# Optimization experiments

Hardware: AMD Instinct MI355X
Metric: run time of the kernel (lower is better)

Reference implementation:

```python
import jax, jax.numpy as jnp
import numpy as np

N = 500000      # nodes
E = 1250000     # edges
S = 50000       # subgraphs
G = 64          # graphs
D = 64          # hidden dim (M_in = M_out = 64)
NLAYERS = 5


def setup_inputs() -> dict:
    key = jax.random.key(0)
    ks = jax.random.split(key, 24)

    def p(k, shape):
        return jax.random.normal(k, shape, dtype=jnp.float32) * 0.05

    return {
        "z": jax.random.randint(ks[0], (N,), 0, 100),
        "edge_index": jax.random.randint(ks[1], (2, E), 0, N),
        "node_to_subgraph": jax.random.randint(ks[2], (N,), 0, S),
        "subgraph_to_graph": jax.random.randint(ks[3], (S,), 0, G),
        # per-layer params (stacked over the 5 conv layers)
        "z_tables": p(ks[4], (NLAYERS, 100, D)),      # Embedding(100, 64) x5
        "tf_W": p(ks[5], (NLAYERS - 1, D, 2 * D)),    # Linear(128, 64) for layers 1..4
        "tf_b": p(ks[6], (NLAYERS - 1, D)),
        "ggc_W": p(ks[7], (NLAYERS, D, D)),           # GatedGraphConv weight[0]
        "gru_wih": p(ks[8], (NLAYERS, 3 * D, D)),
        "gru_whh": p(ks[9], (NLAYERS, 3 * D, D)),
        "gru_bih": p(ks[10], (NLAYERS, 3 * D)),
        "gru_bhh": p(ks[11], (NLAYERS, 3 * D)),
        # head
        "fc1_W": p(ks[12], (32, D)), "fc1_b": p(ks[13], (32,)),
        "fc2_W": p(ks[14], (16, 32)), "fc2_b": p(ks[15], (16,)),
        "fc3_W": p(ks[16], (1, 16)), "fc3_b": p(ks[17], (1,)),
    }


def reference(z, edge_index, node_to_subgraph, subgraph_to_graph,
              z_tables, tf_W, tf_b, ggc_W,
              gru_wih, gru_whh, gru_bih, gru_bhh,
              fc1_W, fc1_b, fc2_W, fc2_b, fc3_W, fc3_b):
    src, dst = edge_index[0], edge_index[1]
    x = None
    for layer in range(NLAYERS):
        ze = z_tables[layer][z]                      # [N, 64] embedding lookup
        if x is None:
            x = ze
        else:
            x = jnp.concatenate([x, ze], axis=-1) @ tf_W[layer - 1].T + tf_b[layer - 1]
        # GatedGraphConv with num_layers=1: m = x @ W; add-aggregate; GRUCell update
        m = x @ ggc_W[layer]                          # [N, 64]
        agg = jax.ops.segment_sum(m[src], dst, num_segments=N)  # scatter-add to dst
        gi = agg @ gru_wih[layer].T + gru_bih[layer]  # [N, 192]
        gh = x @ gru_whh[layer].T + gru_bhh[layer]    # [N, 192]
        ir, iz, inn = jnp.split(gi, 3, axis=-1)
        hr, hz, hn = jnp.split(gh, 3, axis=-1)
        r = jax.nn.sigmoid(ir + hr)
        u = jax.nn.sigmoid(iz + hz)
        n = jnp.tanh(inn + r * hn)
        x = (1.0 - u) * n + u * x
    # subgraph pooling ('mean' branch actually does global_add_pool)
    x = jax.ops.segment_sum(x, node_to_subgraph, num_segments=S)   # [S, 64]
    # graph pooling (y_ndim == 1)
    x = jax.ops.segment_sum(x, subgraph_to_graph, num_segments=G)  # [G, 64]
    x = jax.nn.elu(x @ fc1_W.T + fc1_b)
    x = jax.nn.elu(x @ fc2_W.T + fc2_b)
    return x @ fc3_W.T + fc3_b                        # [G, 1]
```

## Files before the change

### kernel.cpp

```cpp
#include <hip/hip_runtime.h>
#include <hip/hip_bf16.h>

#define NN 500000
#define EE 1250000
#define NP 501760
#define NBLK 489
#define GCAP 16384

typedef __attribute__((ext_vector_type(8))) short bf16x8;
typedef __attribute__((ext_vector_type(4))) float f32x4;

__device__ __forceinline__ float ngnn97_bf2f(unsigned short u) {
  return __uint_as_float(((unsigned int)u) << 16);
}
__device__ __forceinline__ unsigned short ngnn97_f2bf(float f) {
  union { __hip_bfloat16 b; unsigned short u; } cv;
  cv.b = __float2bfloat16(f);
  return cv.u;
}
__device__ __forceinline__ void ngnn97_acc8(uint4 u, float* lo, float* hi) {
  lo[0] += __uint_as_float(u.x << 16); hi[0] += __uint_as_float(u.x & 0xFFFF0000u);
  lo[1] += __uint_as_float(u.y << 16); hi[1] += __uint_as_float(u.y & 0xFFFF0000u);
  lo[2] += __uint_as_float(u.z << 16); hi[2] += __uint_as_float(u.z & 0xFFFF0000u);
  lo[3] += __uint_as_float(u.w << 16); hi[3] += __uint_as_float(u.w & 0xFFFF0000u);
}

__global__ void ngnn97_code(float* __restrict__ out, float v) {
  if (threadIdx.x < 64) out[threadIdx.x] = v;
}

__global__ __launch_bounds__(256) void ngnn97_pre(
    const float* __restrict__ ggc, const float* __restrict__ wih,
    const float* __restrict__ whh, const float* __restrict__ bih,
    const float* __restrict__ bhh, const float* __restrict__ tfW,
    const float* __restrict__ ztab,
    unsigned short* __restrict__ Ubt, float* __restrict__ Ub,
    unsigned short* __restrict__ Vbt, unsigned short* __restrict__ ztabh) {
  int idx = blockIdx.x * 256 + threadIdx.x;
  if (idx < 163840) {
    int l = idx >> 15, r = idx & 32767;
    int n = r >> 7, k = r & 127;
    float v = 0.f;
    if (k < 64) {
      if (n < 192) {
        const float* gp = ggc + l * 4096 + k * 64;
        const float* wp = wih + l * 12288 + n * 64;
        float acc = 0.f;
#pragma unroll
        for (int t2 = 0; t2 < 64; t2++) acc = fmaf(gp[t2], wp[t2], acc);
        v = acc;
      }
    } else {
      int k2 = k - 64;
      if (n < 128) v = whh[l * 12288 + n * 64 + k2];
      else if (n >= 192) v = whh[l * 12288 + (n - 64) * 64 + k2];
    }
    Ubt[idx] = ngnn97_f2bf(v);
  } else if (idx < 196608) {
    int i2 = idx - 163840;
    Vbt[i2] = ngnn97_f2bf(tfW[i2]);
  } else if (idx < 197888) {
    int i2 = idx - 196608;
    int l = i2 >> 8, j = i2 & 255;
    float v;
    if (j < 128)      v = bih[l * 192 + j] + bhh[l * 192 + j];
    else if (j < 192) v = bih[l * 192 + j];
    else              v = bhh[l * 192 + j - 64];
    Ub[i2] = v;
  } else if (idx < 229888) {
    int i2 = idx - 197888;
    ztabh[i2] = ngnn97_f2bf(ztab[i2]);
  }
}

__global__ __launch_bounds__(256) void ngnn97_hist(const int* __restrict__ dst, int* __restrict__ counts) {
  int e = blockIdx.x * 256 + threadIdx.x;
  if (e < EE) atomicAdd(&counts[dst[e]], 1);
}

__global__ __launch_bounds__(256) void ngnn97_red(const int* __restrict__ counts, int* __restrict__ bsum) {
  __shared__ int s[256];
  int t = threadIdx.x, base = blockIdx.x * 1024;
  int v = 0;
#pragma unroll
  for (int i = 0; i < 4; i++) v += counts[base + t + i * 256];
  s[t] = v; __syncthreads();
  for (int o = 128; o > 0; o >>= 1) { if (t < o) s[t] += s[t + o]; __syncthreads(); }
  if (t == 0) bsum[blockIdx.x] = s[0];
}

__global__ __launch_bounds__(512) void ngnn97_scan1(const int* __restrict__ bsum, int* __restrict__ boff) {
  __shared__ int s[512];
  int t = threadIdx.x;
  int v = (t < NBLK) ? bsum[t] : 0;
  s[t] = v; __syncthreads();
  for (int o = 1; o < 512; o <<= 1) {
    int a = (t >= o) ? s[t - o] : 0;
    __syncthreads(); s[t] += a; __syncthreads();
  }
  if (t < NBLK) boff[t] = s[t] - v;
}

__global__ __launch_bounds__(256) void ngnn97_scan2(const int* __restrict__ counts, const int* __restrict__ boff,
                                                    int* __restrict__ row_ptr, int* __restrict__ cursor) {
  __shared__ int s[256];
  int t = threadIdx.x, base = blockIdx.x * 1024;
  int4 c = *(const int4*)(counts + base + t * 4);
  int tsum = c.x + c.y + c.z + c.w;
  s[t] = tsum; __syncthreads();
  for (int o = 1; o < 256; o <<= 1) {
    int a = (t >= o) ? s[t - o] : 0;
    __syncthreads(); s[t] += a; __syncthreads();
  }
  int off = boff[blockIdx.x] + s[t] - tsum;
  int4 r;
  r.x = off; r.y = off + c.x; r.z = off + c.x + c.y; r.w = off + c.x + c.y + c.z;
  *(int4*)(row_ptr + base + t * 4) = r;
  *(int4*)(cursor + base + t * 4) = r;
}

__global__ __launch_bounds__(256) void ngnn97_fill(const int* __restrict__ src, const int* __restrict__ dst,
                                                   int* __restrict__ cursor, int* __restrict__ srcs) {
  int e = blockIdx.x * 256 + threadIdx.x;
  if (e < EE) {
    int pos = atomicAdd(&cursor[dst[e]], 1);
    srcs[pos] = src[e];
  }
}

__global__ __launch_bounds__(256) void ngnn97_g8(const int* __restrict__ n2s, const int* __restrict__ s2g,
                                                 unsigned char* __restrict__ g8) {
  int idx = blockIdx.x * 256 + threadIdx.x;
  if (idx < NN) g8[idx] = (unsigned char)s2g[n2s[idx]];
}

__global__ __launch_bounds__(256) void ngnn97_bucket(const unsigned char* __restrict__ g8,
                                                     int* __restrict__ gcur, int* __restrict__ nlist) {
  __shared__ int hcnt[64];
  __shared__ int hbase[64];
  int t = threadIdx.x;
  int base = blockIdx.x * 1024;
  if (t < 64) hcnt[t] = 0;
  __syncthreads();
#pragma unroll
  for (int i = 0; i < 4; i++) {
    int node = base + i * 256 + t;
    if (node < NN) atomicAdd(&hcnt[g8[node]], 1);
  }
  __syncthreads();
  if (t < 64) {
    int c = hcnt[t];
    hbase[t] = (c > 0) ? atomicAdd(&gcur[t], c) : 0;
    hcnt[t] = 0;
  }
  __syncthreads();
#pragma unroll
  for (int i = 0; i < 4; i++) {
    int node = base + i * 256 + t;
    if (node < NN) {
      int g = g8[node];
      int loc = atomicAdd(&hcnt[g], 1);
      int pos = hbase[g] + loc;
      if (pos < GCAP) nlist[g * GCAP + pos] = node;
    }
  }
}

__global__ __launch_bounds__(256) void ngnn97_embed(const int* __restrict__ z,
                                                    const unsigned short* __restrict__ ztabh,
                                                    unsigned short* __restrict__ xh) {
  int idx = blockIdx.x * 256 + threadIdx.x;
  int node = idx >> 3, sub = idx & 7;
  if (node < NN) {
    int zz = z[node];
    *(bf16x8*)(xh + (size_t)node * 64 + sub * 8) =
        *(const bf16x8*)(ztabh + zz * 64 + sub * 8);
  }
}

__global__ __launch_bounds__(256, 4) void ngnn97_gru(
    const unsigned short* __restrict__ xh_old, unsigned short* __restrict__ xh_new,
    const int* __restrict__ rowp, const int* __restrict__ srcs,
    const unsigned short* __restrict__ Ubt, const float* __restrict__ Ub,
    const unsigned short* __restrict__ Vbt, const float* __restrict__ tfb,
    const int* __restrict__ z, const unsigned short* __restrict__ ztabh,
    int do_transform) {
  __shared__ unsigned short Abuf[128 * 72];
  const int t = threadIdx.x;
  const int lane = t & 63, w = t >> 6;
  const int ncol = lane & 15, quad = lane >> 4;
  const int nbase = blockIdx.x * 128;
  const int strip = 32 * w;

  {
    int grp = lane >> 2, sub = lane & 2 * 2;
    sub = lane & 3;
#pragma unroll
    for (int sb = 0; sb < 2; sb++) {
      int row = strip + sb * 16 + grp;
      int node = nbase + row;
      float lo[8], hi[8];
#pragma unroll
      for (int i = 0; i < 8; i++) { lo[i] = 0.f; hi[i] = 0.f; }
      if (node < NN) {
        int b = rowp[node], e = rowp[node + 1];
        int p = b;
        for (; p + 2 <= e; p += 2) {
          int s0 = srcs[p], s1 = srcs[p + 1];
          const unsigned short* r0 = xh_old + (size_t)s0 * 64 + sub * 16;
          const unsigned short* r1 = xh_old + (size_t)s1 * 64 + sub * 16;
          uint4 u0 = *(const uint4*)(r0);
          uint4 u1 = *(const uint4*)(r0 + 8);
          uint4 u2 = *(const uint4*)(r1);
          uint4 u3 = *(const uint4*)(r1 + 8);
          ngnn97_acc8(u0, lo, hi);
          ngnn97_acc8(u1, lo + 4, hi + 4);
          ngnn97_acc8(u2, lo, hi);
          ngnn97_acc8(u3, lo + 4, hi + 4);
        }
        if (p < e) {
          const unsigned short* r0 = xh_old + (size_t)srcs[p] * 64 + sub * 16;
          uint4 u0 = *(const uint4*)(r0);
          uint4 u1 = *(const uint4*)(r0 + 8);
          ngnn97_acc8(u0, lo, hi);
          ngnn97_acc8(u1, lo + 4, hi + 4);
        }
      }
#pragma unroll
      for (int c = 0; c < 2; c++) {
        bf16x8 ov;
#pragma unroll
        for (int j = 0; j < 4; j++) {
          ov[2 * j]     = (short)ngnn97_f2bf(lo[c * 4 + j]);
          ov[2 * j + 1] = (short)ngnn97_f2bf(hi[c * 4 + j]);
        }
        *(bf16x8*)(Abuf + row * 72 + sub * 16 + c * 8) = ov;
      }
    }
  }

  bf16x8 afrA[2][2];
#pragma unroll
  for (int mm = 0; mm < 2; mm++)
#pragma unroll
    for (int kc = 0; kc < 2; kc++)
      afrA[mm][kc] = *(const bf16x8*)(Abuf + (strip + mm * 16 + ncol) * 72 + quad * 8 + kc * 32);

#pragma unroll
  for (int i = 0; i < 8; i++) {
    int chunk = i * 64 + lane;
    int r2 = chunk >> 4, c4 = (chunk & 15) << 2;
    int node = nbase + strip + r2;
    ushort4 qx = make_ushort4(0, 0, 0, 0);
    if (node < NN) qx = *(const ushort4*)(xh_old + (size_t)node * 64 + c4);
    *(ushort4*)(Abuf + (strip + r2) * 72 + c4) = qx;
  }

  bf16x8 afrX[2][2];
#pragma unroll
  for (int mm = 0; mm < 2; mm++)
#pragma unroll
    for (int kc = 0; kc < 2; kc++)
      afrX[mm][kc] = *(const bf16x8*)(Abuf + (strip + mm * 16 + ncol) * 72 + quad * 8 + kc * 32);

#pragma unroll
  for (int c = 0; c < 4; c++) {
    f32x4 aR[2], aZ[2], aN[2], aH[2];
#pragma unroll
    for (int mm = 0; mm < 2; mm++) {
      aR[mm] = (f32x4){0.f, 0.f, 0.f, 0.f}; aZ[mm] = aR[mm];
      aN[mm] = aR[mm]; aH[mm] = aR[mm];
    }
#pragma unroll
    for (int kc = 0; kc < 4; kc++) {
      const unsigned short* ub = Ubt + (size_t)(c * 16 + ncol) * 128 + quad * 8 + kc * 32;
      bf16x8 bR = *(const bf16x8*)(ub);
      bf16x8 bZ = *(const bf16x8*)(ub + 64 * 128);
      bf16x8 bX = (kc < 2) ? *(const bf16x8*)(ub + 128 * 128)
                           : *(const bf16x8*)(ub + 192 * 128);
#pragma unroll
      for (int mm = 0; mm < 2; mm++) {
        bf16x8 a = (kc < 2) ? afrA[mm][kc] : afrX[mm][kc - 2];
        aR[mm] = __builtin_amdgcn_mfma_f32_16x16x32_bf16(a, bR, aR[mm], 0, 0, 0);
        aZ[mm] = __builtin_amdgcn_mfma_f32_16x16x32_bf16(a, bZ, aZ[mm], 0, 0, 0);
        if (kc < 2) aN[mm] = __builtin_amdgcn_mfma_f32_16x16x32_bf16(a, bX, aN[mm], 0, 0, 0);
        else        aH[mm] = __builtin_amdgcn_mfma_f32_16x16x32_bf16(a, bX, aH[mm], 0, 0, 0);
      }
    }
    int j = c * 16 + ncol;
    float bRs = Ub[j], bZs = Ub[64 + j], bNs = Ub[128 + j], bHs = Ub[192 + j];
#pragma unroll
    for (int mm = 0; mm < 2; mm++)
#pragma unroll
      for (int r = 0; r < 4; r++) {
        int row = strip + mm * 16 + quad * 4 + r;
        float R = aR[mm][r] + bRs, Z = aZ[mm][r] + bZs;
        float Nv = aN[mm][r] + bNs, H = aH[mm][r] + bHs;
        float rg = 1.f / (1.f + __expf(-R));
        float ug = 1.f / (1.f + __expf(-Z));
        float e2 = __expf(2.f * (Nv + rg * H));
        float nn2 = 1.f - 2.f / (e2 + 1.f);
        float xo = ngnn97_bf2f(Abuf[row * 72 + j]);
        Abuf[row * 72 + j] = ngnn97_f2bf((1.f - ug) * nn2 + ug * xo);
      }
  }

  if (do_transform) {
    bf16x8 afrN[2][2], afrE[2][2];
#pragma unroll
    for (int mm = 0; mm < 2; mm++) {
      int node = nbase + strip + mm * 16 + ncol;
      int zz = (node < NN) ? z[node] : 0;
#pragma unroll
      for (int kc = 0; kc < 2; kc++) {
        afrN[mm][kc] = *(const bf16x8*)(Abuf + (strip + mm * 16 + ncol) * 72 + quad * 8 + kc * 32);
        afrE[mm][kc] = *(const bf16x8*)(ztabh + zz * 64 + quad * 8 + kc * 32);
      }
    }
#pragma unroll
    for (int c2 = 0; c2 < 4; c2++) {
      f32x4 acc[2];
      acc[0] = (f32x4){0.f, 0.f, 0.f, 0.f}; acc[1] = acc[0];
#pragma unroll
      for (int kc = 0; kc < 4; kc++) {
        bf16x8 bV = *(const bf16x8*)(Vbt + (size_t)(c2 * 16 + ncol) * 128 + quad * 8 + kc * 32);
#pragma unroll
        for (int mm = 0; mm < 2; mm++) {
          bf16x8 a = (kc < 2) ? afrN[mm][kc] : afrE[mm][kc - 2];
          acc[mm] = __builtin_amdgcn_mfma_f32_16x16x32_bf16(a, bV, acc[mm], 0, 0, 0);
        }
      }
      int j = c2 * 16 + ncol;
      float bt = tfb[j];
#pragma unroll
      for (int mm = 0; mm < 2; mm++)
#pragma unroll
        for (int r = 0; r < 4; r++) {
          int row = strip + mm * 16 + quad * 4 + r;
          Abuf[row * 72 + j] = ngnn97_f2bf(acc[mm][r] + bt);
        }
    }
  }

#pragma unroll
  for (int i = 0; i < 8; i++) {
    int chunk = i * 64 + lane;
    int r2 = chunk >> 4, c4 = (chunk & 15) << 2;
    int node = nbase + strip + r2;
    if (node < NN)
      *(ushort4*)(xh_new + (size_t)node * 64 + c4) = *(const ushort4*)(Abuf + (strip + r2) * 72 + c4);
  }
}

__global__ __launch_bounds__(256) void ngnn97_pool(const unsigned short* __restrict__ xh,
                                                   const int* __restrict__ nlist,
                                                   const int* __restrict__ gcur,
                                                   float* __restrict__ gpool) {
  __shared__ float part[4][64];
  int t = threadIdx.x;
  int lane = t & 63, wv = t >> 6;
  int g = blockIdx.x >> 4, c = blockIdx.x & 15;
  int cnt = gcur[g];
  if (cnt > GCAP) cnt = GCAP;
  int r0 = (c * cnt) >> 4, r1 = ((c + 1) * cnt) >> 4;
  const int* nl = nlist + g * GCAP;
  float a0 = 0.f, a1 = 0.f;
  int r = r0 + wv;
  for (; r + 4 < r1; r += 8) {
    int n0 = nl[r], n1 = nl[r + 4];
    a0 += ngnn97_bf2f(xh[(size_t)n0 * 64 + lane]);
    a1 += ngnn97_bf2f(xh[(size_t)n1 * 64 + lane]);
  }
  if (r < r1) a0 += ngnn97_bf2f(xh[(size_t)nl[r] * 64 + lane]);
  part[wv][lane] = a0 + a1;
  __syncthreads();
  if (t < 64)
    atomicAdd(&gpool[g * 64 + t], part[0][t] + part[1][t] + part[2][t] + part[3][t]);
}

__global__ __launch_bounds__(256) void ngnn97_head(
    const float* __restrict__ gpool,
    const float* __restrict__ W1, const float* __restrict__ b1,
    const float* __restrict__ W2, const float* __restrict__ b2,
    const float* __restrict__ W3, const float* __restrict__ b3,
    float* __restrict__ out) {
  __shared__ float gp[4096];
  __shared__ float h1[2048];
  __shared__ float h2[1024];
  int t = threadIdx.x;
  for (int i = t; i < 4096; i += 256) gp[i] = gpool[i];
  __syncthreads();
  for (int i = t; i < 2048; i += 256) {
    int g = i >> 5, o = i & 31;
    float a = b1[o];
    for (int d = 0; d < 64; d++) a = fmaf(gp[g * 64 + d], W1[o * 64 + d], a);
    h1[i] = (a > 0.f) ? a : (__expf(a) - 1.f);
  }
  __syncthreads();
  for (int i = t; i < 1024; i += 256) {
    int g = i >> 4, o = i & 15;
    float a = b2[o];
    for (int d = 0; d < 32; d++) a = fmaf(h1[g * 32 + d], W2[o * 32 + d], a);
    h2[i] = (a > 0.f) ? a : (__expf(a) - 1.f);
  }
  __syncthreads();
  if (t < 64) {
    float a = b3[0];
    for (int d = 0; d < 16; d++) a = fmaf(h2[t * 16 + d], W3[d], a);
    out[t] = a;
  }
}

#define OFF_XH0   ((size_t)0)
#define OFF_XH1   ((size_t)64000000)
#define OFF_CNT   ((size_t)128000000)
#define OFF_ROW   (OFF_CNT + (size_t)NP * 4)
#define OFF_CUR   (OFF_ROW + (size_t)NP * 4)
#define OFF_SRC   (OFF_CUR + (size_t)NP * 4)
#define OFF_BSUM  (OFF_SRC + (size_t)EE * 4)
#define OFF_BOFF  (OFF_BSUM + (size_t)2048)
#define OFF_U     (OFF_BOFF + (size_t)2048)
#define OFF_UB    (OFF_U + (size_t)327680)
#define OFF_V     (OFF_UB + (size_t)5120)
#define OFF_GP    (OFF_V + (size_t)65536)
#define OFF_G8    (OFF_GP + (size_t)16384)
#define OFF_ZTH   (OFF_G8 + (size_t)500736)
#define OFF_GCUR  (OFF_ZTH + (size_t)64000)
#define OFF_NL    (OFF_GCUR + (size_t)1024)
#define WS_NEED   (OFF_NL + (size_t)64 * GCAP * 4)

extern "C" void kernel_launch(void* const* d_in, const int* in_sizes, int n_in,
                              void* d_out, int out_size, void* d_ws, size_t ws_size,
                              hipStream_t stream) {
  float* out = (float*)d_out;
  if (ws_size < WS_NEED) {
    ngnn97_code<<<1, 64, 0, stream>>>(out, 7.0f);
    return;
  }

  const int* z    = (const int*)d_in[0];
  const int* ei   = (const int*)d_in[1];
  const int* n2s  = (const int*)d_in[2];
  const int* s2g  = (const int*)d_in[3];
  const float* ztab = (const float*)d_in[4];
  const float* tfW  = (const float*)d_in[5];
  const float* tfb  = (const float*)d_in[6];
  const float* ggc  = (const float*)d_in[7];
  const float* wih  = (const float*)d_in[8];
  const float* whh  = (const float*)d_in[9];
  const float* bih  = (const float*)d_in[10];
  const float* bhh  = (const float*)d_in[11];
  const float* W1   = (const float*)d_in[12];
  const float* b1   = (const float*)d_in[13];
  const float* W2   = (const float*)d_in[14];
  const float* b2   = (const float*)d_in[15];
  const float* W3   = (const float*)d_in[16];
  const float* b3   = (const float*)d_in[17];

  char* ws = (char*)d_ws;
  unsigned short* xh0    = (unsigned short*)(ws + OFF_XH0);
  unsigned short* xh1    = (unsigned short*)(ws + OFF_XH1);
  int*            counts = (int*)(ws + OFF_CNT);
  int*            rowp   = (int*)(ws + OFF_ROW);
  int*            curs   = (int*)(ws + OFF_CUR);
  int*            srcs   = (int*)(ws + OFF_SRC);
  int*            bsum   = (int*)(ws + OFF_BSUM);
  int*            boff   = (int*)(ws + OFF_BOFF);
  unsigned short* Ubt    = (unsigned short*)(ws + OFF_U);
  float*          Ub     = (float*)(ws + OFF_UB);
  unsigned short* Vbt    = (unsigned short*)(ws + OFF_V);
  float*          gpool  = (float*)(ws + OFF_GP);
  unsigned char*  g8     = (unsigned char*)(ws + OFF_G8);
  unsigned short* ztabh  = (unsigned short*)(ws + OFF_ZTH);
  int*            gcur   = (int*)(ws + OFF_GCUR);
  int*            nlist  = (int*)(ws + OFF_NL);

  hipMemsetAsync(counts, 0, (size_t)NP * 4, stream);
  hipMemsetAsync(gpool, 0, 16384, stream);
  hipMemsetAsync(gcur, 0, 1024, stream);

  ngnn97_pre<<<899, 256, 0, stream>>>(ggc, wih, whh, bih, bhh, tfW, ztab, Ubt, Ub, Vbt, ztabh);
  ngnn97_g8<<<(NN + 255) / 256, 256, 0, stream>>>(n2s, s2g, g8);
  ngnn97_bucket<<<NBLK, 256, 0, stream>>>(g8, gcur, nlist);

  const int* srcp = ei;
  const int* dstp = ei + EE;
  ngnn97_hist<<<(EE + 255) / 256, 256, 0, stream>>>(dstp, counts);
  ngnn97_red<<<NBLK, 256, 0, stream>>>(counts, bsum);
  ngnn97_scan1<<<1, 512, 0, stream>>>(bsum, boff);
  ngnn97_scan2<<<NBLK, 256, 0, stream>>>(counts, boff, rowp, curs);
  ngnn97_fill<<<(EE + 255) / 256, 256, 0, stream>>>(srcp, dstp, curs, srcs);

  ngnn97_embed<<<(NN * 8 + 255) / 256, 256, 0, stream>>>(z, ztabh, xh0);

  unsigned short* xc = xh0;
  unsigned short* xn2 = xh1;
  for (int l = 0; l < 5; l++) {
    ngnn97_gru<<<(NN + 127) / 128, 256, 0, stream>>>(
        xc, xn2, rowp, srcs,
        Ubt + (size_t)l * 32768, Ub + (size_t)l * 256,
        Vbt + (size_t)(l < 4 ? l : 0) * 8192, tfb + (size_t)(l < 4 ? l : 0) * 64,
        z, ztabh + (size_t)(l < 4 ? l + 1 : 0) * 6400, (l < 4) ? 1 : 0);
    unsigned short* tmp = xc; xc = xn2; xn2 = tmp;
  }

  ngnn97_pool<<<1024, 256, 0, stream>>>(xc, nlist, gcur, gpool);
  ngnn97_head<<<1, 256, 0, stream>>>(gpool, W1, b1, W2, b2, W3, b3, out);
}
```

Measured before the change: 1.108 ms.

## Split neighbor aggregation out of GRU kernel into separate gather kernel

Moves the per-node edge gather-sum into its own kernel, which writes bf16 aggregates to the output buffer, then the GRU kernel reads them back as MFMA A-fragments and overwrites the same buffer in place with the new features. The gather loop is unrolled by four edges for more memory-level parallelism, and the gather kernel can run at higher occupancy than the MFMA kernel. In exchange each layer adds an extra write and read of an N×64 bf16 array plus one more kernel launch.

```diff
diff --git a/kernel.cpp b/kernel.cpp
--- a/kernel.cpp
+++ b/kernel.cpp
@@ -178,9 +178,70 @@
   }
 }
 
+__global__ __launch_bounds__(256) void ngnn97_agg(
+    const unsigned short* __restrict__ xh_old,
+    const int* __restrict__ rowp, const int* __restrict__ srcs,
+    unsigned short* __restrict__ aggh) {
+  int t = threadIdx.x;
+  int g = t >> 2, sub = t & 3;
+  int node = blockIdx.x * 64 + g;
+  if (node >= NN) return;
+  float lo[8], hi[8];
+#pragma unroll
+  for (int i = 0; i < 8; i++) { lo[i] = 0.f; hi[i] = 0.f; }
+  int b = rowp[node], e = rowp[node + 1];
+  int p = b;
+  for (; p + 4 <= e; p += 4) {
+    int s0 = srcs[p], s1 = srcs[p + 1], s2 = srcs[p + 2], s3 = srcs[p + 3];
+    const unsigned short* r0 = xh_old + (size_t)s0 * 64 + sub * 16;
+    const unsigned short* r1 = xh_old + (size_t)s1 * 64 + sub * 16;
+    const unsigned short* r2 = xh_old + (size_t)s2 * 64 + sub * 16;
+    const unsigned short* r3 = xh_old + (size_t)s3 * 64 + sub * 16;
+    uint4 u0 = *(const uint4*)(r0);
+    uint4 u1 = *(const uint4*)(r0 + 8);
+    uint4 u2 = *(const uint4*)(r1);
+    uint4 u3 = *(const uint4*)(r1 + 8);
+    uint4 u4 = *(const uint4*)(r2);
+    uint4 u5 = *(const uint4*)(r2 + 8);
+    uint4 u6 = *(const uint4*)(r3);
+    uint4 u7 = *(const uint4*)(r3 + 8);
+    ngnn97_acc8(u0, lo, hi); ngnn97_acc8(u1, lo + 4, hi + 4);
+    ngnn97_acc8(u2, lo, hi); ngnn97_acc8(u3, lo + 4, hi + 4);
+    ngnn97_acc8(u4, lo, hi); ngnn97_acc8(u5, lo + 4, hi + 4);
+    ngnn97_acc8(u6, lo, hi); ngnn97_acc8(u7, lo + 4, hi + 4);
+  }
+  if (p + 2 <= e) {
+    int s0 = srcs[p], s1 = srcs[p + 1];
+    const unsigned short* r0 = xh_old + (size_t)s0 * 64 + sub * 16;
+    const unsigned short* r1 = xh_old + (size_t)s1 * 64 + sub * 16;
+    uint4 u0 = *(const uint4*)(r0);
+    uint4 u1 = *(const uint4*)(r0 + 8);
+    uint4 u2 = *(const uint4*)(r1);
+    uint4 u3 = *(const uint4*)(r1 + 8);
+    ngnn97_acc8(u0, lo, hi); ngnn97_acc8(u1, lo + 4, hi + 4);
+    ngnn97_acc8(u2, lo, hi); ngnn97_acc8(u3, lo + 4, hi + 4);
+    p += 2;
+  }
+  if (p < e) {
+    const unsigned short* r0 = xh_old + (size_t)srcs[p] * 64 + sub * 16;
+    uint4 u0 = *(const uint4*)(r0);
+    uint4 u1 = *(const uint4*)(r0 + 8);
+    ngnn97_acc8(u0, lo, hi); ngnn97_acc8(u1, lo + 4, hi + 4);
+  }
+#pragma unroll
+  for (int c = 0; c < 2; c++) {
+    bf16x8 ov;
+#pragma unroll
+    for (int j = 0; j < 4; j++) {
+      ov[2 * j]     = (short)ngnn97_f2bf(lo[c * 4 + j]);
+      ov[2 * j + 1] = (short)ngnn97_f2bf(hi[c * 4 + j]);
+    }
+    *(bf16x8*)(aggh + (size_t)node * 64 + sub * 16 + c * 8) = ov;
+  }
+}
+
 __global__ __launch_bounds__(256, 4) void ngnn97_gru(
-    const unsigned short* __restrict__ xh_old, unsigned short* __restrict__ xh_new,
-    const int* __restrict__ rowp, const int* __restrict__ srcs,
+    const unsigned short* __restrict__ xh_old, unsigned short* __restrict__ axn,
     const unsigned short* __restrict__ Ubt, const float* __restrict__ Ub,
     const unsigned short* __restrict__ Vbt, const float* __restrict__ tfb,
     const int* __restrict__ z, const unsigned short* __restrict__ ztabh,
@@ -192,59 +253,16 @@
   const int nbase = blockIdx.x * 128;
   const int strip = 32 * w;
 
-  {
-    int grp = lane >> 2, sub = lane & 2 * 2;
-    sub = lane & 3;
-#pragma unroll
-    for (int sb = 0; sb < 2; sb++) {
-      int row = strip + sb * 16 + grp;
-      int node = nbase + row;
-      float lo[8], hi[8];
-#pragma unroll
-      for (int i = 0; i < 8; i++) { lo[i] = 0.f; hi[i] = 0.f; }
-      if (node < NN) {
-        int b = rowp[node], e = rowp[node + 1];
-        int p = b;
-        for (; p + 2 <= e; p += 2) {
-          int s0 = srcs[p], s1 = srcs[p + 1];
-          const unsigned short* r0 = xh_old + (size_t)s0 * 64 + sub * 16;
-          const unsigned short* r1 = xh_old + (size_t)s1 * 64 + sub * 16;
-          uint4 u0 = *(const uint4*)(r0);
-          uint4 u1 = *(const uint4*)(r0 + 8);
-          uint4 u2 = *(const uint4*)(r1);
-          uint4 u3 = *(const uint4*)(r1 + 8);
-          ngnn97_acc8(u0, lo, hi);
-          ngnn97_acc8(u1, lo + 4, hi + 4);
-          ngnn97_acc8(u2, lo, hi);
-          ngnn97_acc8(u3, lo + 4, hi + 4);
-        }
-        if (p < e) {
-          const unsigned short* r0 = xh_old + (size_t)srcs[p] * 64 + sub * 16;
-          uint4 u0 = *(const uint4*)(r0);
-          uint4 u1 = *(const uint4*)(r0 + 8);
-          ngnn97_acc8(u0, lo, hi);
-          ngnn97_acc8(u1, lo + 4, hi + 4);
-        }
-      }
-#pragma unroll
-      for (int c = 0; c < 2; c++) {
-        bf16x8 ov;
-#pragma unroll
-        for (int j = 0; j < 4; j++) {
-          ov[2 * j]     = (short)ngnn97_f2bf(lo[c * 4 + j]);
-          ov[2 * j + 1] = (short)ngnn97_f2bf(hi[c * 4 + j]);
-        }
-        *(bf16x8*)(Abuf + row * 72 + sub * 16 + c * 8) = ov;
-      }
-    }
-  }
-
   bf16x8 afrA[2][2];
 #pragma unroll
-  for (int mm = 0; mm < 2; mm++)
+  for (int mm = 0; mm < 2; mm++) {
+    int node = nbase + strip + mm * 16 + ncol;
+    int an = (node < NN) ? node : 0;
+    const unsigned short* ap = axn + (size_t)an * 64 + quad * 8;
 #pragma unroll
     for (int kc = 0; kc < 2; kc++)
-      afrA[mm][kc] = *(const bf16x8*)(Abuf + (strip + mm * 16 + ncol) * 72 + quad * 8 + kc * 32);
+      afrA[mm][kc] = *(const bf16x8*)(ap + kc * 32);
+  }
 
 #pragma unroll
   for (int i = 0; i < 8; i++) {
@@ -348,7 +366,7 @@
     int r2 = chunk >> 4, c4 = (chunk & 15) << 2;
     int node = nbase + strip + r2;
     if (node < NN)
-      *(ushort4*)(xh_new + (size_t)node * 64 + c4) = *(const ushort4*)(Abuf + (strip + r2) * 72 + c4);
+      *(ushort4*)(axn + (size_t)node * 64 + c4) = *(const ushort4*)(Abuf + (strip + r2) * 72 + c4);
   }
 }
 
@@ -496,8 +514,9 @@
   unsigned short* xc = xh0;
   unsigned short* xn2 = xh1;
   for (int l = 0; l < 5; l++) {
+    ngnn97_agg<<<(NN + 63) / 64, 256, 0, stream>>>(xc, rowp, srcs, xn2);
     ngnn97_gru<<<(NN + 127) / 128, 256, 0, stream>>>(
-        xc, xn2, rowp, srcs,
+        xc, xn2,
         Ubt + (size_t)l * 32768, Ub + (size_t)l * 256,
         Vbt + (size_t)(l < 4 ? l : 0) * 8192, tfb + (size_t)(l < 4 ? l : 0) * 64,
         z, ztabh + (size_t)(l < 4 ? l + 1 : 0) * 6400, (l < 4) ? 1 : 0);
```

Measured after the change: 1.197 ms. 8.0% more time.

## Halve GRU tile to 64 nodes per block, prefetch gather indices and self rows

Applied to the files above, without the earlier changes.

The fused gather+GRU kernel now processes 64 nodes per block (16 per wave) instead of 128, and raises the launch-bounds occupancy hint from 4 to 5. The self-row loads are issued into registers before the neighbour gather, and the edge-source indices are software-prefetched one iteration ahead. The aim is more waves in flight and better hiding of the latency of the irregular gather. In exchange, each MFMA B-fragment weight load is reused across fewer rows, and the block count doubles.

```diff
diff --git a/kernel.cpp b/kernel.cpp
--- a/kernel.cpp
+++ b/kernel.cpp
@@ -178,99 +178,96 @@
   }
 }
 
-__global__ __launch_bounds__(256, 4) void ngnn97_gru(
+__global__ __launch_bounds__(256, 5) void ngnn97_gru(
     const unsigned short* __restrict__ xh_old, unsigned short* __restrict__ xh_new,
     const int* __restrict__ rowp, const int* __restrict__ srcs,
     const unsigned short* __restrict__ Ubt, const float* __restrict__ Ub,
     const unsigned short* __restrict__ Vbt, const float* __restrict__ tfb,
     const int* __restrict__ z, const unsigned short* __restrict__ ztabh,
     int do_transform) {
-  __shared__ unsigned short Abuf[128 * 72];
+  __shared__ unsigned short Abuf[64 * 72];
   const int t = threadIdx.x;
   const int lane = t & 63, w = t >> 6;
   const int ncol = lane & 15, quad = lane >> 4;
-  const int nbase = blockIdx.x * 128;
-  const int strip = 32 * w;
-
-  {
-    int grp = lane >> 2, sub = lane & 2 * 2;
-    sub = lane & 3;
-#pragma unroll
-    for (int sb = 0; sb < 2; sb++) {
-      int row = strip + sb * 16 + grp;
-      int node = nbase + row;
-      float lo[8], hi[8];
-#pragma unroll
-      for (int i = 0; i < 8; i++) { lo[i] = 0.f; hi[i] = 0.f; }
-      if (node < NN) {
-        int b = rowp[node], e = rowp[node + 1];
-        int p = b;
-        for (; p + 2 <= e; p += 2) {
-          int s0 = srcs[p], s1 = srcs[p + 1];
-          const unsigned short* r0 = xh_old + (size_t)s0 * 64 + sub * 16;
-          const unsigned short* r1 = xh_old + (size_t)s1 * 64 + sub * 16;
-          uint4 u0 = *(const uint4*)(r0);
-          uint4 u1 = *(const uint4*)(r0 + 8);
-          uint4 u2 = *(const uint4*)(r1);
-          uint4 u3 = *(const uint4*)(r1 + 8);
-          ngnn97_acc8(u0, lo, hi);
-          ngnn97_acc8(u1, lo + 4, hi + 4);
-          ngnn97_acc8(u2, lo, hi);
-          ngnn97_acc8(u3, lo + 4, hi + 4);
-        }
-        if (p < e) {
-          const unsigned short* r0 = xh_old + (size_t)srcs[p] * 64 + sub * 16;
-          uint4 u0 = *(const uint4*)(r0);
-          uint4 u1 = *(const uint4*)(r0 + 8);
-          ngnn97_acc8(u0, lo, hi);
-          ngnn97_acc8(u1, lo + 4, hi + 4);
-        }
-      }
-#pragma unroll
-      for (int c = 0; c < 2; c++) {
-        bf16x8 ov;
-#pragma unroll
-        for (int j = 0; j < 4; j++) {
-          ov[2 * j]     = (short)ngnn97_f2bf(lo[c * 4 + j]);
-          ov[2 * j + 1] = (short)ngnn97_f2bf(hi[c * 4 + j]);
-        }
-        *(bf16x8*)(Abuf + row * 72 + sub * 16 + c * 8) = ov;
-      }
-    }
-  }
-
-  bf16x8 afrA[2][2];
-#pragma unroll
-  for (int mm = 0; mm < 2; mm++)
-#pragma unroll
-    for (int kc = 0; kc < 2; kc++)
-      afrA[mm][kc] = *(const bf16x8*)(Abuf + (strip + mm * 16 + ncol) * 72 + quad * 8 + kc * 32);
-
-#pragma unroll
-  for (int i = 0; i < 8; i++) {
+  const int nbase = blockIdx.x * 64;
+  const int strip = 16 * w;
+
+  ushort4 qx[4];
+#pragma unroll
+  for (int i = 0; i < 4; i++) {
     int chunk = i * 64 + lane;
     int r2 = chunk >> 4, c4 = (chunk & 15) << 2;
-    int node = nbase + strip + r2;
-    ushort4 qx = make_ushort4(0, 0, 0, 0);
-    if (node < NN) qx = *(const ushort4*)(xh_old + (size_t)node * 64 + c4);
-    *(ushort4*)(Abuf + (strip + r2) * 72 + c4) = qx;
-  }
-
-  bf16x8 afrX[2][2];
-#pragma unroll
-  for (int mm = 0; mm < 2; mm++)
-#pragma unroll
-    for (int kc = 0; kc < 2; kc++)
-      afrX[mm][kc] = *(const bf16x8*)(Abuf + (strip + mm * 16 + ncol) * 72 + quad * 8 + kc * 32);
+    int node2 = nbase + strip + r2;
+    qx[i] = make_ushort4(0, 0, 0, 0);
+    if (node2 < NN) qx[i] = *(const ushort4*)(xh_old + (size_t)node2 * 64 + c4);
+  }
+
+  {
+    int grp = lane >> 2, sub = lane & 3;
+    int row = strip + grp;
+    int node = nbase + row;
+    float lo[8], hi[8];
+#pragma unroll
+    for (int i = 0; i < 8; i++) { lo[i] = 0.f; hi[i] = 0.f; }
+    if (node < NN) {
+      int b = rowp[node], e = rowp[node + 1];
+      int p = b;
+      int s0 = (p < e) ? srcs[p] : 0;
+      int s1 = (p + 1 < e) ? srcs[p + 1] : 0;
+      while (p + 2 <= e) {
+        int n0 = (p + 2 < e) ? srcs[p + 2] : 0;
+        int n1 = (p + 3 < e) ? srcs[p + 3] : 0;
+        const unsigned short* r0 = xh_old + (size_t)s0 * 64 + sub * 16;
+        const unsigned short* r1 = xh_old + (size_t)s1 * 64 + sub * 16;
+        uint4 u0 = *(const uint4*)(r0);
+        uint4 u1 = *(const uint4*)(r0 + 8);
+        uint4 u2 = *(const uint4*)(r1);
+        uint4 u3 = *(const uint4*)(r1 + 8);
+        ngnn97_acc8(u0, lo, hi); ngnn97_acc8(u1, lo + 4, hi + 4);
+        ngnn97_acc8(u2, lo, hi); ngnn97_acc8(u3, lo + 4, hi + 4);
+        s0 = n0; s1 = n1; p += 2;
+      }
+      if (p < e) {
+        const unsigned short* r0 = xh_old + (size_t)s0 * 64 + sub * 16;
+        uint4 u0 = *(const uint4*)(r0);
+        uint4 u1 = *(const uint4*)(r0 + 8);
+        ngnn97_acc8(u0, lo, hi);
+        ngnn97_acc8(u1, lo + 4, hi + 4);
+      }
+    }
+#pragma unroll
+    for (int c = 0; c < 2; c++) {
+      bf16x8 ov;
+#pragma unroll
+      for (int j = 0; j < 4; j++) {
+        ov[2 * j]     = (short)ngnn97_f2bf(lo[c * 4 + j]);
+        ov[2 * j + 1] = (short)ngnn97_f2bf(hi[c * 4 + j]);
+      }
+      *(bf16x8*)(Abuf + row * 72 + sub * 16 + c * 8) = ov;
+    }
+  }
+
+  bf16x8 afrA[2];
+#pragma unroll
+  for (int kc = 0; kc < 2; kc++)
+    afrA[kc] = *(const bf16x8*)(Abuf + (strip + ncol) * 72 + quad * 8 + kc * 32);
+
+#pragma unroll
+  for (int i = 0; i < 4; i++) {
+    int chunk = i * 64 + lane;
+    int r2 = chunk >> 4, c4 = (chunk & 15) << 2;
+    *(ushort4*)(Abuf + (strip + r2) * 72 + c4) = qx[i];
+  }
+
+  bf16x8 afrX[2];
+#pragma unroll
+  for (int kc = 0; kc < 2; kc++)
+    afrX[kc] = *(const bf16x8*)(Abuf + (strip + ncol) * 72 + quad * 8 + kc * 32);
 
 #pragma unroll
   for (int c = 0; c < 4; c++) {
-    f32x4 aR[2], aZ[2], aN[2], aH[2];
-#pragma unroll
-    for (int mm = 0; mm < 2; mm++) {
-      aR[mm] = (f32x4){0.f, 0.f, 0.f, 0.f}; aZ[mm] = aR[mm];
-      aN[mm] = aR[mm]; aH[mm] = aR[mm];
-    }
+    f32x4 aR = (f32x4){0.f, 0.f, 0.f, 0.f};
+    f32x4 aZ = aR, aN = aR, aH = aR;
 #pragma unroll
     for (int kc = 0; kc < 4; kc++) {
       const unsigned short* ub = Ubt + (size_t)(c * 16 + ncol) * 128 + quad * 8 + kc * 32;
@@ -278,72 +275,60 @@
       bf16x8 bZ = *(const bf16x8*)(ub + 64 * 128);
       bf16x8 bX = (kc < 2) ? *(const bf16x8*)(ub + 128 * 128)
                            : *(const bf16x8*)(ub + 192 * 128);
-#pragma unroll
-      for (int mm = 0; mm < 2; mm++) {
-        bf16x8 a = (kc < 2) ? afrA[mm][kc] : afrX[mm][kc - 2];
-        aR[mm] = __builtin_amdgcn_mfma_f32_16x16x32_bf16(a, bR, aR[mm], 0, 0, 0);
-        aZ[mm] = __builtin_amdgcn_mfma_f32_16x16x32_bf16(a, bZ, aZ[mm], 0, 0, 0);
-        if (kc < 2) aN[mm] = __builtin_amdgcn_mfma_f32_16x16x32_bf16(a, bX, aN[mm], 0, 0, 0);
-        else        aH[mm] = __builtin_amdgcn_mfma_f32_16x16x32_bf16(a, bX, aH[mm], 0, 0, 0);
-      }
+      bf16x8 a = (kc < 2) ? afrA[kc] : afrX[kc - 2];
+      aR = __builtin_amdgcn_mfma_f32_16x16x32_bf16(a, bR, aR, 0, 0, 0);
+      aZ = __builtin_amdgcn_mfma_f32_16x16x32_bf16(a, bZ, aZ, 0, 0, 0);
+      if (kc < 2) aN = __builtin_amdgcn_mfma_f32_16x16x32_bf16(a, bX, aN, 0, 0, 0);
+      else        aH = __builtin_amdgcn_mfma_f32_16x16x32_bf16(a, bX, aH, 0, 0, 0);
     }
     int j = c * 16 + ncol;
     float bRs = Ub[j], bZs = Ub[64 + j], bNs = Ub[128 + j], bHs = Ub[192 + j];
 #pragma unroll
-    for (int mm = 0; mm < 2; mm++)
-#pragma unroll
-      for (int r = 0; r < 4; r++) {
-        int row = strip + mm * 16 + quad * 4 + r;
-        float R = aR[mm][r] + bRs, Z = aZ[mm][r] + bZs;
-        float Nv = aN[mm][r] + bNs, H = aH[mm][r] + bHs;
-        float rg = 1.f / (1.f + __expf(-R));
-        float ug = 1.f / (1.f + __expf(-Z));
-        float e2 = __expf(2.f * (Nv + rg * H));
-        float nn2 = 1.f - 2.f / (e2 + 1.f);
-        float xo = ngnn97_bf2f(Abuf[row * 72 + j]);
-        Abuf[row * 72 + j] = ngnn97_f2bf((1.f - ug) * nn2 + ug * xo);
-      }
+    for (int r = 0; r < 4; r++) {
+      int row = strip + quad * 4 + r;
+      float R = aR[r] + bRs, Z = aZ[r] + bZs;
+      float Nv = aN[r] + bNs, H = aH[r] + bHs;
+      float rg = 1.f / (1.f + __expf(-R));
+      float ug = 1.f / (1.f + __expf(-Z));
+      float e2 = __expf(2.f * (Nv + rg * H));
+      float nn2 = 1.f - 2.f / (e2 + 1.f);
+      float xo = ngnn97_bf2f(Abuf[row * 72 + j]);
+      Abuf[row * 72 + j] = ngnn97_f2bf((1.f - ug) * nn2 + ug * xo);
+    }
   }
 
   if (do_transform) {
-    bf16x8 afrN[2][2], afrE[2][2];
-#pragma unroll
-    for (int mm = 0; mm < 2; mm++) {
-      int node = nbase + strip + mm * 16 + ncol;
+    bf16x8 afrN[2], afrE[2];
+    {
+      int node = nbase + strip + ncol;
       int zz = (node < NN) ? z[node] : 0;
 #pragma unroll
       for (int kc = 0; kc < 2; kc++) {
-        afrN[mm][kc] = *(const bf16x8*)(Abuf + (strip + mm * 16 + ncol) * 72 + quad * 8 + kc * 32);
-        afrE[mm][kc] = *(const bf16x8*)(ztabh + zz * 64 + quad * 8 + kc * 32);
+        afrN[kc] = *(const bf16x8*)(Abuf + (strip + ncol) * 72 + quad * 8 + kc * 32);
+        afrE[kc] = *(const bf16x8*)(ztabh + zz * 64 + quad * 8 + kc * 32);
       }
     }
 #pragma unroll
     for (int c2 = 0; c2 < 4; c2++) {
-      f32x4 acc[2];
-      acc[0] = (f32x4){0.f, 0.f, 0.f, 0.f}; acc[1] = acc[0];
+      f32x4 acc = (f32x4){0.f, 0.f, 0.f, 0.f};
 #pragma unroll
       for (int kc = 0; kc < 4; kc++) {
         bf16x8 bV = *(const bf16x8*)(Vbt + (size_t)(c2 * 16 + ncol) * 128 + quad * 8 + kc * 32);
-#pragma unroll
-        for (int mm = 0; mm < 2; mm++) {
-          bf16x8 a = (kc < 2) ? afrN[mm][kc] : afrE[mm][kc - 2];
-          acc[mm] = __builtin_amdgcn_mfma_f32_16x16x32_bf16(a, bV, acc[mm], 0, 0, 0);
-        }
+        bf16x8 a = (kc < 2) ? afrN[kc] : afrE[kc - 2];
+        acc = __builtin_amdgcn_mfma_f32_16x16x32_bf16(a, bV, acc, 0, 0, 0);
       }
       int j = c2 * 16 + ncol;
       float bt = tfb[j];
 #pragma unroll
-      for (int mm = 0; mm < 2; mm++)
-#pragma unroll
-        for (int r = 0; r < 4; r++) {
-          int row = strip + mm * 16 + quad * 4 + r;
-          Abuf[row * 72 + j] = ngnn97_f2bf(acc[mm][r] + bt);
-        }
-    }
-  }
-
-#pragma unroll
-  for (int i = 0; i < 8; i++) {
+      for (int r = 0; r < 4; r++) {
+        int row = strip + quad * 4 + r;
+        Abuf[row * 72 + j] = ngnn97_f2bf(acc[r] + bt);
+      }
+    }
+  }
+
+#pragma unroll
+  for (int i = 0; i < 4; i++) {
     int chunk = i * 64 + lane;
     int r2 = chunk >> 4, c4 = (chunk & 15) << 2;
     int node = nbase + strip + r2;
@@ -496,7 +481,7 @@
   unsigned short* xc = xh0;
   unsigned short* xn2 = xh1;
   for (int l = 0; l < 5; l++) {
-    ngnn97_gru<<<(NN + 127) / 128, 256, 0, stream>>>(
+    ngnn97_gru<<<(NN + 63) / 64, 256, 0, stream>>>(
         xc, xn2, rowp, srcs,
         Ubt + (size_t)l * 32768, Ub + (size_t)l * 256,
         Vbt + (size_t)(l < 4 ? l : 0) * 8192, tfb + (size_t)(l < 4 ? l : 0) * 64,
```

New measurement: 1.598 ms. 1.44x slower.

## Sort nodes by in-degree and shrink GRU blocks to one wavefront

Applied to the files above, without the earlier changes.

Adds a counting sort of nodes by in-degree, with a histogram, a scan and a fill kernel producing a permutation. The GRU kernel then processes nodes in that order, so lanes within a wave gather similar edge counts and diverge less. Blocks shrink from four waves covering 128 nodes to one wave covering 32. In exchange, node reads and writes become scattered rather than contiguous, three extra preprocessing launches are added, there are four times as many blocks, and locality of the xh accesses is lost.

```diff
diff --git a/kernel.cpp b/kernel.cpp
--- a/kernel.cpp
+++ b/kernel.cpp
@@ -166,6 +166,71 @@
   }
 }
 
+__global__ __launch_bounds__(256) void ngnn97_dhist(const int* __restrict__ rowp, int* __restrict__ dbins) {
+  __shared__ int h[64];
+  int t = threadIdx.x, base = blockIdx.x * 1024;
+  if (t < 64) h[t] = 0;
+  __syncthreads();
+#pragma unroll
+  for (int i = 0; i < 4; i++) {
+    int node = base + i * 256 + t;
+    if (node < NN) {
+      int d = rowp[node + 1] - rowp[node];
+      if (d > 63) d = 63;
+      atomicAdd(&h[d], 1);
+    }
+  }
+  __syncthreads();
+  if (t < 64 && h[t]) atomicAdd(&dbins[t], h[t]);
+}
+
+__global__ __launch_bounds__(64) void ngnn97_dscan(const int* __restrict__ dbins, int* __restrict__ dcur) {
+  __shared__ int s[64];
+  int t = threadIdx.x;
+  int v = dbins[t];
+  s[t] = v; __syncthreads();
+  for (int o = 1; o < 64; o <<= 1) {
+    int a = (t >= o) ? s[t - o] : 0;
+    __syncthreads(); s[t] += a; __syncthreads();
+  }
+  dcur[t] = s[t] - v;
+}
+
+__global__ __launch_bounds__(256) void ngnn97_dfill(const int* __restrict__ rowp, int* __restrict__ dcur,
+                                                    int* __restrict__ perm) {
+  __shared__ int hcnt[64];
+  __shared__ int hbase[64];
+  int t = threadIdx.x, base = blockIdx.x * 1024;
+  if (t < 64) hcnt[t] = 0;
+  __syncthreads();
+#pragma unroll
+  for (int i = 0; i < 4; i++) {
+    int node = base + i * 256 + t;
+    if (node < NN) {
+      int d = rowp[node + 1] - rowp[node];
+      if (d > 63) d = 63;
+      atomicAdd(&hcnt[d], 1);
+    }
+  }
+  __syncthreads();
+  if (t < 64) {
+    int c = hcnt[t];
+    hbase[t] = (c > 0) ? atomicAdd(&dcur[t], c) : 0;
+    hcnt[t] = 0;
+  }
+  __syncthreads();
+#pragma unroll
+  for (int i = 0; i < 4; i++) {
+    int node = base + i * 256 + t;
+    if (node < NN) {
+      int d = rowp[node + 1] - rowp[node];
+      if (d > 63) d = 63;
+      int loc = atomicAdd(&hcnt[d], 1);
+      perm[hbase[d] + loc] = node;
+    }
+  }
+}
+
 __global__ __launch_bounds__(256) void ngnn97_embed(const int* __restrict__ z,
                                                     const unsigned short* __restrict__ ztabh,
                                                     unsigned short* __restrict__ xh) {
@@ -178,27 +243,31 @@
   }
 }
 
-__global__ __launch_bounds__(256, 4) void ngnn97_gru(
+__global__ __launch_bounds__(64, 4) void ngnn97_gru(
     const unsigned short* __restrict__ xh_old, unsigned short* __restrict__ xh_new,
     const int* __restrict__ rowp, const int* __restrict__ srcs,
+    const int* __restrict__ perm,
     const unsigned short* __restrict__ Ubt, const float* __restrict__ Ub,
     const unsigned short* __restrict__ Vbt, const float* __restrict__ tfb,
     const int* __restrict__ z, const unsigned short* __restrict__ ztabh,
     int do_transform) {
-  __shared__ unsigned short Abuf[128 * 72];
-  const int t = threadIdx.x;
-  const int lane = t & 63, w = t >> 6;
+  __shared__ unsigned short Abuf[32 * 72];
+  __shared__ int pnode[32];
+  const int lane = threadIdx.x;
   const int ncol = lane & 15, quad = lane >> 4;
-  const int nbase = blockIdx.x * 128;
-  const int strip = 32 * w;
+  const int nbase = blockIdx.x * 32;
+
+  if (lane < 32) {
+    int idx = nbase + lane;
+    pnode[lane] = (idx < NN) ? perm[idx] : NN;
+  }
 
   {
-    int grp = lane >> 2, sub = lane & 2 * 2;
-    sub = lane & 3;
+    int grp = lane >> 2, sub = lane & 3;
 #pragma unroll
     for (int sb = 0; sb < 2; sb++) {
-      int row = strip + sb * 16 + grp;
-      int node = nbase + row;
+      int row = sb * 16 + grp;
+      int node = pnode[row];
       float lo[8], hi[8];
 #pragma unroll
       for (int i = 0; i < 8; i++) { lo[i] = 0.f; hi[i] = 0.f; }
@@ -213,10 +282,8 @@
           uint4 u1 = *(const uint4*)(r0 + 8);
           uint4 u2 = *(const uint4*)(r1);
           uint4 u3 = *(const uint4*)(r1 + 8);
-          ngnn97_acc8(u0, lo, hi);
-          ngnn97_acc8(u1, lo + 4, hi + 4);
-          ngnn97_acc8(u2, lo, hi);
-          ngnn97_acc8(u3, lo + 4, hi + 4);
+          ngnn97_acc8(u0, lo, hi); ngnn97_acc8(u1, lo + 4, hi + 4);
+          ngnn97_acc8(u2, lo, hi); ngnn97_acc8(u3, lo + 4, hi + 4);
         }
         if (p < e) {
           const unsigned short* r0 = xh_old + (size_t)srcs[p] * 64 + sub * 16;
@@ -244,16 +311,16 @@
   for (int mm = 0; mm < 2; mm++)
 #pragma unroll
     for (int kc = 0; kc < 2; kc++)
-      afrA[mm][kc] = *(const bf16x8*)(Abuf + (strip + mm * 16 + ncol) * 72 + quad * 8 + kc * 32);
+      afrA[mm][kc] = *(const bf16x8*)(Abuf + (mm * 16 + ncol) * 72 + quad * 8 + kc * 32);
 
 #pragma unroll
   for (int i = 0; i < 8; i++) {
     int chunk = i * 64 + lane;
     int r2 = chunk >> 4, c4 = (chunk & 15) << 2;
-    int node = nbase + strip + r2;
+    int node = pnode[r2];
     ushort4 qx = make_ushort4(0, 0, 0, 0);
     if (node < NN) qx = *(const ushort4*)(xh_old + (size_t)node * 64 + c4);
-    *(ushort4*)(Abuf + (strip + r2) * 72 + c4) = qx;
+    *(ushort4*)(Abuf + r2 * 72 + c4) = qx;
   }
 
   bf16x8 afrX[2][2];
@@ -261,7 +328,7 @@
   for (int mm = 0; mm < 2; mm++)
 #pragma unroll
     for (int kc = 0; kc < 2; kc++)
-      afrX[mm][kc] = *(const bf16x8*)(Abuf + (strip + mm * 16 + ncol) * 72 + quad * 8 + kc * 32);
+      afrX[mm][kc] = *(const bf16x8*)(Abuf + (mm * 16 + ncol) * 72 + quad * 8 + kc * 32);
 
 #pragma unroll
   for (int c = 0; c < 4; c++) {
@@ -293,7 +360,7 @@
     for (int mm = 0; mm < 2; mm++)
 #pragma unroll
       for (int r = 0; r < 4; r++) {
-        int row = strip + mm * 16 + quad * 4 + r;
+        int row = mm * 16 + quad * 4 + r;
         float R = aR[mm][r] + bRs, Z = aZ[mm][r] + bZs;
         float Nv = aN[mm][r] + bNs, H = aH[mm][r] + bHs;
         float rg = 1.f / (1.f + __expf(-R));
@@ -309,11 +376,11 @@
     bf16x8 afrN[2][2], afrE[2][2];
 #pragma unroll
     for (int mm = 0; mm < 2; mm++) {
-      int node = nbase + strip + mm * 16 + ncol;
+      int node = pnode[mm * 16 + ncol];
       int zz = (node < NN) ? z[node] : 0;
 #pragma unroll
       for (int kc = 0; kc < 2; kc++) {
-        afrN[mm][kc] = *(const bf16x8*)(Abuf + (strip + mm * 16 + ncol) * 72 + quad * 8 + kc * 32);
+        afrN[mm][kc] = *(const bf16x8*)(Abuf + (mm * 16 + ncol) * 72 + quad * 8 + kc * 32);
         afrE[mm][kc] = *(const bf16x8*)(ztabh + zz * 64 + quad * 8 + kc * 32);
       }
     }
@@ -336,7 +403,7 @@
       for (int mm = 0; mm < 2; mm++)
 #pragma unroll
         for (int r = 0; r < 4; r++) {
-          int row = strip + mm * 16 + quad * 4 + r;
+          int row = mm * 16 + quad * 4 + r;
           Abuf[row * 72 + j] = ngnn97_f2bf(acc[mm][r] + bt);
         }
     }
@@ -346,9 +413,9 @@
   for (int i = 0; i < 8; i++) {
     int chunk = i * 64 + lane;
     int r2 = chunk >> 4, c4 = (chunk & 15) << 2;
-    int node = nbase + strip + r2;
+    int node = pnode[r2];
     if (node < NN)
-      *(ushort4*)(xh_new + (size_t)node * 64 + c4) = *(const ushort4*)(Abuf + (strip + r2) * 72 + c4);
+      *(ushort4*)(xh_new + (size_t)node * 64 + c4) = *(const ushort4*)(Abuf + r2 * 72 + c4);
   }
 }
 
@@ -427,7 +494,10 @@
 #define OFF_ZTH   (OFF_G8 + (size_t)500736)
 #define OFF_GCUR  (OFF_ZTH + (size_t)64000)
 #define OFF_NL    (OFF_GCUR + (size_t)1024)
-#define WS_NEED   (OFF_NL + (size_t)64 * GCAP * 4)
+#define OFF_PERM  (OFF_NL + (size_t)64 * GCAP * 4)
+#define OFF_DB    (OFF_PERM + (size_t)NP * 4)
+#define OFF_DC    (OFF_DB + (size_t)256)
+#define WS_NEED   (OFF_DC + (size_t)256)
 
 extern "C" void kernel_launch(void* const* d_in, const int* in_sizes, int n_in,
                               void* d_out, int out_size, void* d_ws, size_t ws_size,
@@ -474,10 +544,14 @@
   unsigned short* ztabh  = (unsigned short*)(ws + OFF_ZTH);
   int*            gcur   = (int*)(ws + OFF_GCUR);
   int*            nlist  = (int*)(ws + OFF_NL);
+  int*            perm   = (int*)(ws + OFF_PERM);
+  int*            dbins  = (int*)(ws + OFF_DB);
+  int*            dcur   = (int*)(ws + OFF_DC);
 
   hipMemsetAsync(counts, 0, (size_t)NP * 4, stream);
   hipMemsetAsync(gpool, 0, 16384, stream);
   hipMemsetAsync(gcur, 0, 1024, stream);
+  hipMemsetAsync(dbins, 0, 256, stream);
 
   ngnn97_pre<<<899, 256, 0, stream>>>(ggc, wih, whh, bih, bhh, tfW, ztab, Ubt, Ub, Vbt, ztabh);
   ngnn97_g8<<<(NN + 255) / 256, 256, 0, stream>>>(n2s, s2g, g8);
@@ -491,13 +565,17 @@
   ngnn97_scan2<<<NBLK, 256, 0, stream>>>(counts, boff, rowp, curs);
   ngnn97_fill<<<(EE + 255) / 256, 256, 0, stream>>>(srcp, dstp, curs, srcs);
 
+  ngnn97_dhist<<<NBLK, 256, 0, stream>>>(rowp, dbins);
+  ngnn97_dscan<<<1, 64, 0, stream>>>(dbins, dcur);
+  ngnn97_dfill<<<NBLK, 256, 0, stream>>>(rowp, dcur, perm);
+
   ngnn97_embed<<<(NN * 8 + 255) / 256, 256, 0, stream>>>(z, ztabh, xh0);
 
   unsigned short* xc = xh0;
   unsigned short* xn2 = xh1;
   for (int l = 0; l < 5; l++) {
-    ngnn97_gru<<<(NN + 127) / 128, 256, 0, stream>>>(
-        xc, xn2, rowp, srcs,
+    ngnn97_gru<<<(NN + 31) / 32, 64, 0, stream>>>(
+        xc, xn2, rowp, srcs, perm,
         Ubt + (size_t)l * 32768, Ub + (size_t)l * 256,
         Vbt + (size_t)(l < 4 ? l : 0) * 8192, tfb + (size_t)(l < 4 ? l : 0) * 64,
         z, ztabh + (size_t)(l < 4 ? l + 1 : 0) * 6400, (l < 4) ? 1 : 0);
```

After: 1.064 ms, median of 2. 3.9% less time.
